# Kernel tuning notes

Measured on AMD Instinct MI355X. Metric: run time of the kernel, lower is better.

## Reference

```python
import jax, jax.numpy as jnp
import numpy as np

B, L, D, H = 2, 2048, 1024, 16
DH = D // H  # 64 per-head depth


def setup_inputs() -> dict:
    key = jax.random.key(0)
    k1, k2, k3 = jax.random.split(key, 3)
    queries = jax.random.normal(k1, (B, L, D), dtype=jnp.float32)
    bias = jnp.zeros((B, 1, 1, L), dtype=jnp.float32)
    w_qkv = jax.random.normal(k2, (D, 3 * D), dtype=jnp.float32) * (D ** -0.5)
    w_o = jax.random.normal(k3, (D, D), dtype=jnp.float32) * (D ** -0.5)
    return {"queries": queries, "bias": bias, "w_qkv": w_qkv, "w_o": w_o}


def _split_heads(x):
    # [B, L, D] -> [B, H, L, DH]
    b, l, d = x.shape
    return x.reshape(b, l, H, d // H).transpose(0, 2, 1, 3)


def reference(queries, bias, w_qkv, w_o):
    # qkv projection (self-attention path, Linear without bias)
    qkv = jnp.einsum("bld,de->ble", queries, w_qkv)
    q, k, v = jnp.split(qkv, [D, 2 * D], axis=-1)
    q = _split_heads(q) * (DH ** -0.5)   # [B,H,Lq,DH]
    k = _split_heads(k)                  # [B,H,Lk,DH]
    v = _split_heads(v)                  # [B,H,Lk,DH]
    logits = jnp.einsum("bhqd,bhkd->bhqk", q, k) + bias
    weights = jax.nn.softmax(logits, axis=-1)  # [B,H,Lq,Lk]
    align = weights.transpose(0, 1, 3, 2)      # [B,H,Lk,Lq]
    # dropout_rate=0 (eval): identity
    context = jnp.einsum("bhqk,bhkd->bhqd", weights, v)
    x = context.transpose(0, 2, 1, 3).reshape(B, L, D)  # combine heads
    out = jnp.einsum("bld,de->ble", x, w_o)
    return out, align
```

## Files before the change

kernel.cpp:

```cpp
#include <hip/hip_runtime.h>

#define BB 2
#define LL 2048
#define DD 1024
#define HH 16
#define DHD 64

typedef __attribute__((ext_vector_type(8))) short bf16x8;
typedef __attribute__((ext_vector_type(4))) float f32x4;
typedef unsigned long long ull;
typedef unsigned short u16;
typedef unsigned int u32;

#define MFMA16(a, b, c) __builtin_amdgcn_mfma_f32_16x16x32_bf16((a), (b), (c), 0, 0, 0)

__device__ __forceinline__ u16 f2bf(float f) {
    union { float f; u32 u; } c; c.f = f;
    u32 r = 0x7FFFu + ((c.u >> 16) & 1u);
    return (u16)((c.u + r) >> 16);
}
__device__ __forceinline__ ull pack4(float x, float y, float z, float w) {
    return (ull)f2bf(x) | ((ull)f2bf(y) << 16) | ((ull)f2bf(z) << 32) | ((ull)f2bf(w) << 48);
}

__device__ __forceinline__ int swz(int row, int col) {
    int key = (row ^ (row >> 3)) & 7;
    return (row << 7) + ((col << 1) ^ (key << 4));
}

__device__ __forceinline__ void gl_lds16(const void* g, void* l) {
    __builtin_amdgcn_global_load_lds(
        (const __attribute__((address_space(1))) u32*)g,
        (__attribute__((address_space(3))) u32*)l, 16, 0, 0);
}

__global__ __launch_bounds__(256) void to_bf16(const float* __restrict__ in,
                                               u16* __restrict__ out, int n4) {
    int i = blockIdx.x * 256 + threadIdx.x;
    if (i < n4) {
        float4 f = ((const float4*)in)[i];
        ((ull*)out)[i] = pack4(f.x, f.y, f.z, f.w);
    }
}

__global__ __launch_bounds__(256) void transpose_bf16(const float* __restrict__ in,
                                                      u16* __restrict__ out,
                                                      int rows, int cols) {
    __shared__ float t[32][33];
    int bx = blockIdx.x * 32;
    int by = blockIdx.y * 32;
    int tx = threadIdx.x & 31, ty = threadIdx.x >> 5;
#pragma unroll
    for (int i = 0; i < 4; ++i)
        t[ty + i * 8][tx] = in[(size_t)(by + ty + i * 8) * cols + bx + tx];
    __syncthreads();
#pragma unroll
    for (int i = 0; i < 4; ++i)
        out[(size_t)(bx + ty + i * 8) * rows + by + tx] = f2bf(t[tx][ty + i * 8]);
}

template <int BF16OUT>
__global__ __launch_bounds__(256) void gemm_bt(
    const u16* __restrict__ A, const u16* __restrict__ Bt, void* __restrict__ Cout,
    int M, int N, int K)
{
    __shared__ u16 As[128 * 64];
    __shared__ u16 Bs[128 * 64];
    const int tid  = threadIdx.x;
    const int lane = tid & 63, wave = tid >> 6;
    const int l15  = lane & 15, quad = lane >> 4;
    const int m0 = blockIdx.y * 128, n0 = blockIdx.x * 128;
    const int wm = (wave >> 1) * 64, wn = (wave & 1) * 64;

    f32x4 acc[4][4];
#pragma unroll
    for (int i = 0; i < 4; ++i)
#pragma unroll
        for (int j = 0; j < 4; ++j) acc[i][j] = (f32x4){0.f, 0.f, 0.f, 0.f};

    for (int k0 = 0; k0 < K; k0 += 64) {
#pragma unroll
        for (int i = 0; i < 4; ++i) {
            int ci  = (i * 4 + wave) * 64 + lane;
            int row = ci >> 3, c = (ci & 7) * 8;
            gl_lds16(&A[(size_t)(m0 + row) * K + k0 + c],
                     (char*)As + (i * 4 + wave) * 1024);
            gl_lds16(&Bt[(size_t)(n0 + row) * K + k0 + c],
                     (char*)Bs + (i * 4 + wave) * 1024);
        }
        __syncthreads();
#pragma unroll
        for (int ks = 0; ks < 64; ks += 32) {
            bf16x8 a[4], b[4];
#pragma unroll
            for (int i = 0; i < 4; ++i)
                a[i] = *(const bf16x8*)&As[(wm + i * 16 + l15) * 64 + ks + quad * 8];
#pragma unroll
            for (int j = 0; j < 4; ++j)
                b[j] = *(const bf16x8*)&Bs[(wn + j * 16 + l15) * 64 + ks + quad * 8];
#pragma unroll
            for (int i = 0; i < 4; ++i)
#pragma unroll
                for (int j = 0; j < 4; ++j)
                    acc[i][j] = MFMA16(a[i], b[j], acc[i][j]);
        }
        __syncthreads();
    }
#pragma unroll
    for (int i = 0; i < 4; ++i)
#pragma unroll
        for (int j = 0; j < 4; ++j)
#pragma unroll
            for (int r = 0; r < 4; ++r) {
                int row = m0 + wm + i * 16 + quad * 4 + r;
                int col = n0 + wn + j * 16 + l15;
                if (BF16OUT)
                    ((u16*)Cout)[(size_t)row * N + col] = f2bf(acc[i][j][r]);
                else
                    ((float*)Cout)[(size_t)row * N + col] = acc[i][j][r];
            }
}

__global__ __launch_bounds__(256, 4) void attn_v2(
    const u16* __restrict__ qkv,
    const float* __restrict__ bias,
    float* __restrict__ align_out,
    u16* __restrict__ ctx_out)
{
    __shared__ u16 smem[20480];
    u16* QP = smem;
    u16* Ks = smem + 4096;
    u16* Vt = smem + 12288;

    const int tid  = threadIdx.x;
    const int lane = tid & 63, wave = tid >> 6;
    const int l15  = lane & 15, quad = lane >> 4;
    const int strip = wave * 16;
    const int bid = ((blockIdx.x & 7) << 7) | (blockIdx.x >> 3);
    const int bh = bid >> 5, qt = bid & 31;
    const int b  = bh >> 4, h = bh & 15;
    const int q0 = qt * 64;
    const u16* qbase = qkv + (size_t)b * LL * (3 * DD);
    const float scale = 0.125f;

#pragma unroll
    for (int i = 0; i < 2; ++i) {
        int ci  = (i * 4 + wave) * 64 + lane;
        int row = ci >> 3, c = ci & 7;
        int cs  = c ^ ((row ^ (row >> 3)) & 7);
        gl_lds16(&qbase[(size_t)(q0 + row) * (3 * DD) + h * DHD + cs * 8],
                 (char*)QP + (i * 4 + wave) * 1024);
    }
    __syncthreads();
    bf16x8 aq0 = *(const bf16x8*)((const char*)QP + swz(strip + l15, quad * 8));
    bf16x8 aq1 = *(const bf16x8*)((const char*)QP + swz(strip + l15, 32 + quad * 8));

    auto stageK = [&](int kt, int bi) {
#pragma unroll
        for (int i = 0; i < 2; ++i) {
            int ci  = (i * 4 + wave) * 64 + lane;
            int row = ci >> 3, c = ci & 7;
            int cs  = c ^ ((row ^ (row >> 3)) & 7);
            gl_lds16(&qbase[(size_t)(kt * 64 + row) * (3 * DD) + DD + h * DHD + cs * 8],
                     (char*)(Ks + bi * 4096) + (i * 4 + wave) * 1024);
        }
    };

    float m_[4], l_[4];
#pragma unroll
    for (int r = 0; r < 4; ++r) { m_[r] = -1e30f; l_[r] = 0.f; }

    stageK(0, 0);
    __syncthreads();
    for (int kt = 0; kt < 32; ++kt) {
        const int cur = kt & 1;
        if (kt < 31) stageK(kt + 1, cur ^ 1);
        const char* kb = (const char*)(Ks + cur * 4096);
        float Sv[4][4];
#pragma unroll
        for (int j = 0; j < 4; ++j) {
            f32x4 s = (f32x4){0.f, 0.f, 0.f, 0.f};
            bf16x8 bk0 = *(const bf16x8*)(kb + swz(j * 16 + l15, quad * 8));
            bf16x8 bk1 = *(const bf16x8*)(kb + swz(j * 16 + l15, 32 + quad * 8));
            s = MFMA16(aq0, bk0, s);
            s = MFMA16(aq1, bk1, s);
            float bv = bias[b * LL + kt * 64 + j * 16 + l15];
#pragma unroll
            for (int r = 0; r < 4; ++r) Sv[j][r] = s[r] * scale + bv;
        }
#pragma unroll
        for (int r = 0; r < 4; ++r) {
            float tm = fmaxf(fmaxf(Sv[0][r], Sv[1][r]), fmaxf(Sv[2][r], Sv[3][r]));
#pragma unroll
            for (int off = 1; off < 16; off <<= 1) tm = fmaxf(tm, __shfl_xor(tm, off));
            float ts = 0.f;
#pragma unroll
            for (int j = 0; j < 4; ++j) ts += __expf(Sv[j][r] - tm);
#pragma unroll
            for (int off = 1; off < 16; off <<= 1) ts += __shfl_xor(ts, off);
            float mn = fmaxf(m_[r], tm);
            l_[r] = l_[r] * __expf(m_[r] - mn) + ts * __expf(tm - mn);
            m_[r] = mn;
        }
        __syncthreads();
    }

    float rl[4];
#pragma unroll
    for (int r = 0; r < 4; ++r) rl[r] = 1.f / l_[r];
    f32x4 ctx[4];
#pragma unroll
    for (int j = 0; j < 4; ++j) ctx[j] = (f32x4){0.f, 0.f, 0.f, 0.f};

    u16* Pa = QP;

    const int vr0 = tid >> 3, vs0 = tid & 7;
    const int vr1 = (tid + 256) >> 3, vs1 = (tid + 256) & 7;
    const u16* vbase = qbase + 2 * DD + h * DHD;
    bf16x8 vv0, vv1;
    auto loadV = [&](int kt) {
        vv0 = *(const bf16x8*)&vbase[(size_t)(kt * 64 + vr0) * (3 * DD) + vs0 * 8];
        vv1 = *(const bf16x8*)&vbase[(size_t)(kt * 64 + vr1) * (3 * DD) + vs1 * 8];
    };
    auto writeV = [&](int bi) {
        u16* vb = Vt + bi * 4096;
#pragma unroll
        for (int e = 0; e < 8; ++e)
            *(u16*)((char*)vb + swz(vs0 * 8 + e, vr0)) = (u16)vv0[e];
#pragma unroll
        for (int e = 0; e < 8; ++e)
            *(u16*)((char*)vb + swz(vs1 * 8 + e, vr1)) = (u16)vv1[e];
    };

    stageK(0, 0);
    loadV(0);
    writeV(0);
    __syncthreads();
    for (int kt = 0; kt < 32; ++kt) {
        const int cur = kt & 1;
        if (kt < 31) { stageK(kt + 1, cur ^ 1); loadV(kt + 1); }

        const char* kb = (const char*)(Ks + cur * 4096);
        float Sv[4][4];
#pragma unroll
        for (int j = 0; j < 4; ++j) {
            f32x4 s = (f32x4){0.f, 0.f, 0.f, 0.f};
            bf16x8 bk0 = *(const bf16x8*)(kb + swz(j * 16 + l15, quad * 8));
            bf16x8 bk1 = *(const bf16x8*)(kb + swz(j * 16 + l15, 32 + quad * 8));
            s = MFMA16(aq0, bk0, s);
            s = MFMA16(aq1, bk1, s);
            float bv = bias[b * LL + kt * 64 + j * 16 + l15];
#pragma unroll
            for (int r = 0; r < 4; ++r) Sv[j][r] = s[r] * scale + bv;
        }
#pragma unroll
        for (int j = 0; j < 4; ++j) {
            f32x4 pv;
#pragma unroll
            for (int r = 0; r < 4; ++r) {
                float p = __expf(Sv[j][r] - m_[r]) * rl[r];
                pv[r] = p;
                *(u16*)((char*)Pa + swz(strip + quad * 4 + r, j * 16 + l15)) = f2bf(p);
            }
            *(f32x4*)&align_out[((size_t)bh * LL + kt * 64 + j * 16 + l15) * LL +
                                q0 + strip + quad * 4] = pv;
        }
        __syncthreads();
#pragma unroll
        for (int ks = 0; ks < 64; ks += 32) {
            bf16x8 ap = *(const bf16x8*)((const char*)Pa + swz(strip + l15, ks + quad * 8));
            const char* vb = (const char*)(Vt + cur * 4096);
#pragma unroll
            for (int j = 0; j < 4; ++j) {
                bf16x8 bvv = *(const bf16x8*)(vb + swz(j * 16 + l15, ks + quad * 8));
                ctx[j] = MFMA16(ap, bvv, ctx[j]);
            }
        }
        if (kt < 31) writeV(cur ^ 1);
        __syncthreads();
    }

#pragma unroll
    for (int j = 0; j < 4; ++j)
#pragma unroll
        for (int r = 0; r < 4; ++r) {
            int ql = strip + quad * 4 + r;
            int dv = j * 16 + l15;
            ctx_out[(size_t)(b * LL + q0 + ql) * DD + h * DHD + dv] = f2bf(ctx[j][r]);
        }
}

extern "C" void kernel_launch(void* const* d_in, const int* in_sizes, int n_in,
                              void* d_out, int out_size, void* d_ws, size_t ws_size,
                              hipStream_t stream) {
    const float* queries = (const float*)d_in[0];
    const float* bias    = (const float*)d_in[1];
    const float* w_qkv   = (const float*)d_in[2];
    const float* w_o     = (const float*)d_in[3];

    float* out_p   = (float*)d_out;
    float* align_p = out_p + (size_t)BB * LL * DD;

    u16* qbf   = (u16*)d_ws;
    u16* wqkT  = qbf + (size_t)BB * LL * DD;
    u16* woT   = wqkT + (size_t)(3 * DD) * DD;
    u16* qkvbf = woT + (size_t)DD * DD;
    u16* ctxbf = qkvbf + (size_t)BB * LL * 3 * DD;

    to_bf16<<<(BB * LL * DD / 4 + 255) / 256, 256, 0, stream>>>(queries, qbf, BB * LL * DD / 4);
    transpose_bf16<<<dim3(3 * DD / 32, DD / 32), 256, 0, stream>>>(w_qkv, wqkT, DD, 3 * DD);
    transpose_bf16<<<dim3(DD / 32, DD / 32), 256, 0, stream>>>(w_o, woT, DD, DD);

    gemm_bt<1><<<dim3(3 * DD / 128, BB * LL / 128), 256, 0, stream>>>(
        qbf, wqkT, qkvbf, BB * LL, 3 * DD, DD);

    attn_v2<<<dim3(BB * HH * (LL / 64)), 256, 0, stream>>>(qkvbf, bias, align_p, ctxbf);

    gemm_bt<0><<<dim3(DD / 128, BB * LL / 128), 256, 0, stream>>>(
        ctxbf, woT, out_p, BB * LL, DD, DD);
}
```

Before: 777.9 us.

## Double query tile per attention block and defer softmax row reductions

Each attention block now handles 128 queries, 32 per wave, so every K and V tile staged in LDS feeds twice as many MFMAs and global K/V traffic halves. The first pass keeps per-lane running max and sum and merges them across the 16 lanes only once at the end, instead of doing shuffle reductions on every key tile. P is written to LDS as packed 64-bit stores with a permuted column order that matches a permuted V layout. The cost is more registers and LDS per block, fewer blocks in the grid, and dropping the occupancy hint in launch_bounds.

Measured after the change: 746.3 us. -4.1%, faster.

```diff
diff --git a/kernel.cpp b/kernel.cpp
--- a/kernel.cpp
+++ b/kernel.cpp
@@ -121,30 +121,30 @@
             }
 }
 
-__global__ __launch_bounds__(256, 4) void attn_v2(
+__global__ __launch_bounds__(256) void attn_v3(
     const u16* __restrict__ qkv,
     const float* __restrict__ bias,
     float* __restrict__ align_out,
     u16* __restrict__ ctx_out)
 {
-    __shared__ u16 smem[20480];
+    __shared__ u16 smem[24576];
     u16* QP = smem;
-    u16* Ks = smem + 4096;
-    u16* Vt = smem + 12288;
+    u16* Ks = smem + 8192;
+    u16* Vt = smem + 16384;
 
     const int tid  = threadIdx.x;
     const int lane = tid & 63, wave = tid >> 6;
     const int l15  = lane & 15, quad = lane >> 4;
-    const int strip = wave * 16;
-    const int bid = ((blockIdx.x & 7) << 7) | (blockIdx.x >> 3);
-    const int bh = bid >> 5, qt = bid & 31;
+    const int wq   = wave * 32;
+    const int bid = ((blockIdx.x & 7) << 6) | (blockIdx.x >> 3);
+    const int bh = bid >> 4, qt = bid & 15;
     const int b  = bh >> 4, h = bh & 15;
-    const int q0 = qt * 64;
+    const int q0 = qt * 128;
     const u16* qbase = qkv + (size_t)b * LL * (3 * DD);
     const float scale = 0.125f;
 
 #pragma unroll
-    for (int i = 0; i < 2; ++i) {
+    for (int i = 0; i < 4; ++i) {
         int ci  = (i * 4 + wave) * 64 + lane;
         int row = ci >> 3, c = ci & 7;
         int cs  = c ^ ((row ^ (row >> 3)) & 7);
@@ -152,8 +152,12 @@
                  (char*)QP + (i * 4 + wave) * 1024);
     }
     __syncthreads();
-    bf16x8 aq0 = *(const bf16x8*)((const char*)QP + swz(strip + l15, quad * 8));
-    bf16x8 aq1 = *(const bf16x8*)((const char*)QP + swz(strip + l15, 32 + quad * 8));
+    bf16x8 aq[2][2];
+#pragma unroll
+    for (int s = 0; s < 2; ++s) {
+        aq[s][0] = *(const bf16x8*)((const char*)QP + swz(wq + s * 16 + l15, quad * 8));
+        aq[s][1] = *(const bf16x8*)((const char*)QP + swz(wq + s * 16 + l15, 32 + quad * 8));
+    }
 
     auto stageK = [&](int kt, int bi) {
 #pragma unroll
@@ -166,9 +170,11 @@
         }
     };
 
-    float m_[4], l_[4];
-#pragma unroll
-    for (int r = 0; r < 4; ++r) { m_[r] = -1e30f; l_[r] = 0.f; }
+    float m_[2][4], l_[2][4];
+#pragma unroll
+    for (int s = 0; s < 2; ++s)
+#pragma unroll
+        for (int r = 0; r < 4; ++r) { m_[s][r] = -3e38f; l_[s][r] = 0.f; }
 
     stageK(0, 0);
     __syncthreads();
@@ -176,46 +182,67 @@
         const int cur = kt & 1;
         if (kt < 31) stageK(kt + 1, cur ^ 1);
         const char* kb = (const char*)(Ks + cur * 4096);
-        float Sv[4][4];
+        float Sv[2][4][4];
 #pragma unroll
         for (int j = 0; j < 4; ++j) {
-            f32x4 s = (f32x4){0.f, 0.f, 0.f, 0.f};
             bf16x8 bk0 = *(const bf16x8*)(kb + swz(j * 16 + l15, quad * 8));
             bf16x8 bk1 = *(const bf16x8*)(kb + swz(j * 16 + l15, 32 + quad * 8));
-            s = MFMA16(aq0, bk0, s);
-            s = MFMA16(aq1, bk1, s);
             float bv = bias[b * LL + kt * 64 + j * 16 + l15];
 #pragma unroll
-            for (int r = 0; r < 4; ++r) Sv[j][r] = s[r] * scale + bv;
-        }
+            for (int s = 0; s < 2; ++s) {
+                f32x4 sa = (f32x4){0.f, 0.f, 0.f, 0.f};
+                sa = MFMA16(aq[s][0], bk0, sa);
+                sa = MFMA16(aq[s][1], bk1, sa);
+#pragma unroll
+                for (int r = 0; r < 4; ++r) Sv[s][j][r] = sa[r] * scale + bv;
+            }
+        }
+#pragma unroll
+        for (int s = 0; s < 2; ++s)
+#pragma unroll
+            for (int r = 0; r < 4; ++r) {
+                float tm = fmaxf(fmaxf(Sv[s][0][r], Sv[s][1][r]),
+                                 fmaxf(Sv[s][2][r], Sv[s][3][r]));
+                if (tm > m_[s][r]) {
+                    l_[s][r] *= __expf(m_[s][r] - tm);
+                    m_[s][r] = tm;
+                }
+                l_[s][r] += __expf(Sv[s][0][r] - m_[s][r]) + __expf(Sv[s][1][r] - m_[s][r]) +
+                            __expf(Sv[s][2][r] - m_[s][r]) + __expf(Sv[s][3][r] - m_[s][r]);
+            }
+        __syncthreads();
+    }
+
+    float rl[2][4];
+#pragma unroll
+    for (int s = 0; s < 2; ++s)
 #pragma unroll
         for (int r = 0; r < 4; ++r) {
-            float tm = fmaxf(fmaxf(Sv[0][r], Sv[1][r]), fmaxf(Sv[2][r], Sv[3][r]));
-#pragma unroll
-            for (int off = 1; off < 16; off <<= 1) tm = fmaxf(tm, __shfl_xor(tm, off));
-            float ts = 0.f;
-#pragma unroll
-            for (int j = 0; j < 4; ++j) ts += __expf(Sv[j][r] - tm);
-#pragma unroll
-            for (int off = 1; off < 16; off <<= 1) ts += __shfl_xor(ts, off);
-            float mn = fmaxf(m_[r], tm);
-            l_[r] = l_[r] * __expf(m_[r] - mn) + ts * __expf(tm - mn);
-            m_[r] = mn;
-        }
-        __syncthreads();
-    }
-
-    float rl[4];
-#pragma unroll
-    for (int r = 0; r < 4; ++r) rl[r] = 1.f / l_[r];
-    f32x4 ctx[4];
-#pragma unroll
-    for (int j = 0; j < 4; ++j) ctx[j] = (f32x4){0.f, 0.f, 0.f, 0.f};
+            float mv = m_[s][r], lv = l_[s][r];
+#pragma unroll
+            for (int off = 1; off < 16; off <<= 1) {
+                float om = __shfl_xor(mv, off);
+                float ol = __shfl_xor(lv, off);
+                float mn = fmaxf(mv, om);
+                lv = lv * __expf(mv - mn) + ol * __expf(om - mn);
+                mv = mn;
+            }
+            m_[s][r] = mv;
+            rl[s][r] = 1.f / lv;
+        }
+
+    f32x4 ctx[2][4];
+#pragma unroll
+    for (int s = 0; s < 2; ++s)
+#pragma unroll
+        for (int j = 0; j < 4; ++j) ctx[s][j] = (f32x4){0.f, 0.f, 0.f, 0.f};
 
     u16* Pa = QP;
 
     const int vr0 = tid >> 3, vs0 = tid & 7;
-    const int vr1 = (tid + 256) >> 3, vs1 = (tid + 256) & 7;
+    const int vr1 = 32 + (tid >> 3), vs1 = tid & 7;
+    const int p0c = (vr0 & 15) * 4 + (vr0 >> 4);
+    const int p1c = (vr1 & 15) * 4 + (vr1 >> 4);
     const u16* vbase = qbase + 2 * DD + h * DHD;
     bf16x8 vv0, vv1;
     auto loadV = [&](int kt) {
@@ -226,10 +253,10 @@
         u16* vb = Vt + bi * 4096;
 #pragma unroll
         for (int e = 0; e < 8; ++e)
-            *(u16*)((char*)vb + swz(vs0 * 8 + e, vr0)) = (u16)vv0[e];
+            *(u16*)((char*)vb + swz(vs0 * 8 + e, p0c)) = (u16)vv0[e];
 #pragma unroll
         for (int e = 0; e < 8; ++e)
-            *(u16*)((char*)vb + swz(vs1 * 8 + e, vr1)) = (u16)vv1[e];
+            *(u16*)((char*)vb + swz(vs1 * 8 + e, p1c)) = (u16)vv1[e];
     };
 
     stageK(0, 0);
@@ -241,39 +268,55 @@
         if (kt < 31) { stageK(kt + 1, cur ^ 1); loadV(kt + 1); }
 
         const char* kb = (const char*)(Ks + cur * 4096);
-        float Sv[4][4];
+        float Sv[2][4][4];
 #pragma unroll
         for (int j = 0; j < 4; ++j) {
-            f32x4 s = (f32x4){0.f, 0.f, 0.f, 0.f};
             bf16x8 bk0 = *(const bf16x8*)(kb + swz(j * 16 + l15, quad * 8));
             bf16x8 bk1 = *(const bf16x8*)(kb + swz(j * 16 + l15, 32 + quad * 8));
-            s = MFMA16(aq0, bk0, s);
-            s = MFMA16(aq1, bk1, s);
             float bv = bias[b * LL + kt * 64 + j * 16 + l15];
 #pragma unroll
-            for (int r = 0; r < 4; ++r) Sv[j][r] = s[r] * scale + bv;
-        }
-#pragma unroll
-        for (int j = 0; j < 4; ++j) {
-            f32x4 pv;
+            for (int s = 0; s < 2; ++s) {
+                f32x4 sa = (f32x4){0.f, 0.f, 0.f, 0.f};
+                sa = MFMA16(aq[s][0], bk0, sa);
+                sa = MFMA16(aq[s][1], bk1, sa);
+#pragma unroll
+                for (int r = 0; r < 4; ++r) Sv[s][j][r] = sa[r] * scale + bv;
+            }
+        }
+#pragma unroll
+        for (int s = 0; s < 2; ++s) {
+            float p[4][4];
+#pragma unroll
+            for (int j = 0; j < 4; ++j) {
+                f32x4 pv;
+#pragma unroll
+                for (int r = 0; r < 4; ++r) {
+                    pv[r] = __expf(Sv[s][j][r] - m_[s][r]) * rl[s][r];
+                    p[j][r] = pv[r];
+                }
+                *(f32x4*)&align_out[((size_t)bh * LL + kt * 64 + j * 16 + l15) * LL +
+                                    q0 + wq + s * 16 + quad * 4] = pv;
+            }
 #pragma unroll
             for (int r = 0; r < 4; ++r) {
-                float p = __expf(Sv[j][r] - m_[r]) * rl[r];
-                pv[r] = p;
-                *(u16*)((char*)Pa + swz(strip + quad * 4 + r, j * 16 + l15)) = f2bf(p);
-            }
-            *(f32x4*)&align_out[((size_t)bh * LL + kt * 64 + j * 16 + l15) * LL +
-                                q0 + strip + quad * 4] = pv;
+                ull w = pack4(p[0][r], p[1][r], p[2][r], p[3][r]);
+                int row = wq + s * 16 + quad * 4 + r;
+                int k7 = (row ^ (row >> 3)) & 7;
+                *(ull*)((char*)Pa + (row << 7) + ((((l15 >> 1) << 4) ^ (k7 << 4))) +
+                        ((l15 & 1) << 3)) = w;
+            }
         }
         __syncthreads();
 #pragma unroll
         for (int ks = 0; ks < 64; ks += 32) {
-            bf16x8 ap = *(const bf16x8*)((const char*)Pa + swz(strip + l15, ks + quad * 8));
             const char* vb = (const char*)(Vt + cur * 4096);
+            bf16x8 ap0 = *(const bf16x8*)((const char*)Pa + swz(wq + l15, ks + quad * 8));
+            bf16x8 ap1 = *(const bf16x8*)((const char*)Pa + swz(wq + 16 + l15, ks + quad * 8));
 #pragma unroll
             for (int j = 0; j < 4; ++j) {
                 bf16x8 bvv = *(const bf16x8*)(vb + swz(j * 16 + l15, ks + quad * 8));
-                ctx[j] = MFMA16(ap, bvv, ctx[j]);
+                ctx[0][j] = MFMA16(ap0, bvv, ctx[0][j]);
+                ctx[1][j] = MFMA16(ap1, bvv, ctx[1][j]);
             }
         }
         if (kt < 31) writeV(cur ^ 1);
@@ -281,13 +324,15 @@
     }
 
 #pragma unroll
-    for (int j = 0; j < 4; ++j)
-#pragma unroll
-        for (int r = 0; r < 4; ++r) {
-            int ql = strip + quad * 4 + r;
-            int dv = j * 16 + l15;
-            ctx_out[(size_t)(b * LL + q0 + ql) * DD + h * DHD + dv] = f2bf(ctx[j][r]);
-        }
+    for (int s = 0; s < 2; ++s)
+#pragma unroll
+        for (int j = 0; j < 4; ++j)
+#pragma unroll
+            for (int r = 0; r < 4; ++r) {
+                int ql = wq + s * 16 + quad * 4 + r;
+                int dv = j * 16 + l15;
+                ctx_out[(size_t)(b * LL + q0 + ql) * DD + h * DHD + dv] = f2bf(ctx[s][j][r]);
+            }
 }
 
 extern "C" void kernel_launch(void* const* d_in, const int* in_sizes, int n_in,
@@ -314,7 +359,7 @@
     gemm_bt<1><<<dim3(3 * DD / 128, BB * LL / 128), 256, 0, stream>>>(
         qbf, wqkT, qkvbf, BB * LL, 3 * DD, DD);
 
-    attn_v2<<<dim3(BB * HH * (LL / 64)), 256, 0, stream>>>(qkvbf, bias, align_p, ctxbf);
+    attn_v3<<<dim3(BB * HH * (LL / 128)), 256, 0, stream>>>(qkvbf, bias, align_p, ctxbf);
 
     gemm_bt<0><<<dim3(DD / 128, BB * LL / 128), 256, 0, stream>>>(
         ctxbf, woT, out_p, BB * LL, DD, DD);
```
